# Kernel tuning notes

Measured on AMD Instinct MI355X. Metric: run time of the kernel, lower is better.

Reference implementation:

```python
import jax, jax.numpy as jnp
import numpy as np

B, T, D_IN = 8192, 32, 2
EMB, H = 128, 256


def setup_inputs() -> dict:
    key = jax.random.key(0)
    ks = jax.random.split(key, 8)
    s = 0.05
    return {
        "traj_inputs": jax.random.normal(ks[0], (B, T, D_IN), dtype=jnp.float32),
        "W_emb": jax.random.normal(ks[1], (D_IN, EMB), dtype=jnp.float32) * s,
        "b_emb": jnp.zeros((EMB,), dtype=jnp.float32),
        "W0": jax.random.normal(ks[2], (EMB, 4 * H), dtype=jnp.float32) * s,
        "U0": jax.random.normal(ks[3], (H, 4 * H), dtype=jnp.float32) * s,
        "b0": jnp.zeros((4 * H,), dtype=jnp.float32),
        "W1": jax.random.normal(ks[4], (H, 4 * H), dtype=jnp.float32) * s,
        "U1": jax.random.normal(ks[5], (H, 4 * H), dtype=jnp.float32) * s,
        "b1": jnp.zeros((4 * H,), dtype=jnp.float32),
    }


def _lstm_layer(x_seq, W, U, b):
    # x_seq: [B, T, D]; Keras LSTMCell gate order i, f, g(c), o
    bsz = x_seq.shape[0]
    h0 = jnp.zeros((bsz, H), dtype=x_seq.dtype)
    c0 = jnp.zeros((bsz, H), dtype=x_seq.dtype)
    # precompute input projection for all timesteps (one big GEMM)
    xz = jnp.einsum("btd,dk->btk", x_seq, W) + b  # [B, T, 4H]

    def step(carry, xz_t):
        h, c = carry
        z = xz_t + h @ U
        i, f, g, o = jnp.split(z, 4, axis=-1)
        i = jax.nn.sigmoid(i)
        f = jax.nn.sigmoid(f)
        g = jnp.tanh(g)
        o = jax.nn.sigmoid(o)
        c = f * c + i * g
        h = o * jnp.tanh(c)
        return (h, c), h

    (h_f, c_f), ys = jax.lax.scan(step, (h0, c0), jnp.swapaxes(xz, 0, 1))
    return jnp.swapaxes(ys, 0, 1), h_f, c_f  # [B,T,H], [B,H], [B,H]


def reference(traj_inputs, W_emb, b_emb, W0, U0, b0, W1, U1, b1):
    # position embedding: Dense(emb_size, relu)
    x = jax.nn.relu(traj_inputs @ W_emb + b_emb)  # [B, T, EMB]
    # stacked 2-layer LSTM, return_sequences + return_state
    y0, h0, c0 = _lstm_layer(x, W0, U0, b0)
    y1, h1, c1 = _lstm_layer(y0, W1, U1, b1)
    # Keras RNN(StackedRNNCells) returns (seq_out, [h0,c0], [h1,c1])
    return y1, h0, c0, h1, c1
```

## Files before the change

### kernel.cpp

```cpp
#include <hip/hip_runtime.h>
#include <hip/hip_bf16.h>


typedef __attribute__((ext_vector_type(8))) __bf16 bf16x8;
typedef __attribute__((ext_vector_type(4))) __bf16 bf16x4;
typedef __attribute__((ext_vector_type(4))) float f32x4;

#define MFMA16(a, b, c) __builtin_amdgcn_mfma_f32_16x16x32_bf16(a, b, c, 0, 0, 0)

#define WAIT_VM7() __builtin_amdgcn_s_waitcnt(0xF77)
#define WAIT_LGKM0() __builtin_amdgcn_s_waitcnt(0xC07F)
#define RAW_BARRIER()                  \
  do {                                 \
    WAIT_LGKM0();                      \
    __builtin_amdgcn_sched_barrier(0); \
    __builtin_amdgcn_s_barrier();      \
  } while (0)

__device__ __forceinline__ float fexp2(float x) {
#if __has_builtin(__builtin_amdgcn_exp2f)
  return __builtin_amdgcn_exp2f(x);
#else
  return exp2f(x);
#endif
}
__device__ __forceinline__ float frcp(float x) {
#if __has_builtin(__builtin_amdgcn_rcpf)
  return __builtin_amdgcn_rcpf(x);
#else
  return 1.0f / x;
#endif
}
__device__ __forceinline__ float fsig(float x) {
  return frcp(1.0f + fexp2(-1.44269504f * x));
}
__device__ __forceinline__ float ftanh(float x) {
  return 1.0f - 2.0f * frcp(1.0f + fexp2(2.88539008f * x));
}

__global__ void prep_w0(const float* __restrict__ W0, const float* __restrict__ U0,
                        __bf16* __restrict__ o) {
  const int f = blockIdx.x * 256 + threadIdx.x;
  const int j = f & 7, l5 = (f >> 3) & 63, g = f >> 9;
  const int kc = g % 12, q = (g / 12) & 3, wid = g / 48;
  const int k = (kc << 5) + ((l5 >> 4) << 3) + j;
  const int c = (q << 8) + ((wid >> 2) << 6) + ((wid & 3) << 4) + (l5 & 15);
  const float v = (k < 128) ? W0[(k << 10) + c] : U0[((k - 128) << 10) + c];
  o[f] = (__bf16)v;
}
__global__ void prep_w1(const float* __restrict__ W1, const float* __restrict__ U1,
                        __bf16* __restrict__ o) {
  const int f = blockIdx.x * 256 + threadIdx.x;
  const int j = f & 7, l5 = (f >> 3) & 63, g = f >> 9;
  const int kcx = g & 15, q = (g >> 4) & 3, wid = g >> 6;
  const int k = (kcx << 5) + ((l5 >> 4) << 3) + j;
  const int c = (q << 8) + ((wid >> 2) << 6) + ((wid & 3) << 4) + (l5 & 15);
  const float v = (k < 256) ? W1[(k << 10) + c] : U1[((k - 256) << 10) + c];
  o[f] = (__bf16)v;
}

__global__ __launch_bounds__(1024)
void lstm_l0(const float* __restrict__ traj,
             const float* __restrict__ Wemb,
             const float* __restrict__ bemb,
             const float* __restrict__ bias0,
             const __bf16* __restrict__ wb0,
             float* __restrict__ out,
             __bf16* __restrict__ slab) {
  __shared__ float s_We[384];
  __shared__ float s_traj[2048];
  __shared__ __bf16 s_h0[8192];
  __shared__ __bf16 s_ring[65536];

  const int tid = threadIdx.x;
  const int wid = tid >> 6;
  const int l = tid & 63;
  const int lr = l & 15, lg = l >> 4;
  const int w = wid >> 2, s4 = wid & 3;
  const int xr = (lr & 7) << 3;
  const int r0 = blockIdx.x << 5;
  const int e0 = (w << 6) + (s4 << 4) + (lg << 2);

  if (tid < 384) s_We[tid] = (tid < 256) ? Wemb[tid] : bemb[tid - 256];
  for (int i = tid; i < 2048; i += 1024) {
    const int r = i >> 6, tt = (i >> 1) & 31, d = i & 1;
    s_traj[(tt << 6) + (r << 1) + d] = traj[(r0 << 6) + i];
  }
  for (int i = tid; i < 8192; i += 1024) s_h0[i] = (__bf16)0.f;
  __syncthreads();

  float c0s[2][4] = {};
  const __bf16* wp0 = wb0 + wid * 48 * 512 + l * 8;
  __bf16* ringp = &s_ring[wid << 12];

  auto stage = [&](int cf) {
    const __bf16* src = wp0 + (((cf & 3) * 12 + (cf >> 2)) << 9);
    __builtin_amdgcn_global_load_lds(
        (const __attribute__((address_space(1))) void*)src,
        (__attribute__((address_space(3))) void*)(ringp + ((cf & 7) << 9)),
        16, 0, 0);
  };
  auto ring_read = [&](int cf) {
    return *reinterpret_cast<const bf16x8*>(ringp + ((cf & 7) << 9) + (l << 3));
  };

  stage(0); stage(1); stage(2); stage(3); stage(4); stage(5); stage(6);

#pragma unroll 1
  for (int t = 0; t < 32; ++t) {
    f32x4 acc[4][2];
#pragma unroll
    for (int q = 0; q < 4; ++q) {
      const f32x4 bq = *reinterpret_cast<const f32x4*>(bias0 + (q << 8) + e0);
      acc[q][0] = bq;
      acc[q][1] = bq;
    }
    float t0v[2], t1v[2];
#pragma unroll
    for (int rt = 0; rt < 2; ++rt) {
      const int r = (rt << 4) + lr;
      t0v[rt] = s_traj[(t << 6) + (r << 1)];
      t1v[rt] = s_traj[(t << 6) + (r << 1) + 1];
    }
#pragma unroll
    for (int kc = 0; kc < 12; ++kc) {
      bf16x8 ia[2];
      if (kc < 4) {
#pragma unroll
        for (int rt = 0; rt < 2; ++rt) {
#pragma unroll
          for (int j = 0; j < 8; ++j) {
            const int k = (kc << 5) + (lg << 3) + j;
            const float x = fmaf(t0v[rt], s_We[k],
                                 fmaf(t1v[rt], s_We[128 + k], s_We[256 + k]));
            ia[rt][j] = (__bf16)fmaxf(x, 0.f);
          }
        }
      } else {
#pragma unroll
        for (int rt = 0; rt < 2; ++rt) {
          const int r = (rt << 4) + lr;
          ia[rt] = *reinterpret_cast<const bf16x8*>(
              &s_h0[(r << 8) + ((((kc - 4) << 5) + (lg << 3)) ^ xr)]);
        }
      }
#pragma unroll
      for (int q = 0; q < 4; ++q) {
        const int cf = (kc << 2) + q;
        stage((cf + 7) % 48);
        WAIT_VM7();
        __builtin_amdgcn_sched_barrier(0);
        const bf16x8 wf = ring_read(cf);
        acc[q][0] = MFMA16(wf, ia[0], acc[q][0]);
        acc[q][1] = MFMA16(wf, ia[1], acc[q][1]);
      }
    }
    RAW_BARRIER();
#pragma unroll
    for (int rt = 0; rt < 2; ++rt) {
      const int r = (rt << 4) + lr;
      bf16x4 hv;
      f32x4 cfv;
#pragma unroll
      for (int i = 0; i < 4; ++i) {
        const float cc = fsig(acc[1][rt][i]) * c0s[rt][i] +
                         fsig(acc[0][rt][i]) * ftanh(acc[2][rt][i]);
        c0s[rt][i] = cc;
        hv[i] = (__bf16)(fsig(acc[3][rt][i]) * ftanh(cc));
        cfv[i] = cc;
      }
      *reinterpret_cast<bf16x4*>(&s_h0[(r << 8) + (e0 ^ xr)]) = hv;
      if (t == 31) {
        *reinterpret_cast<f32x4*>(out + 69206016 + ((r0 + r) << 8) + e0) = cfv;
      }
    }
    RAW_BARRIER();

#pragma unroll
    for (int rr = 0; rr < 2; ++rr) {
      const int row = (wid << 1) + rr;
      const bf16x4 hv4 = *reinterpret_cast<const bf16x4*>(
          &s_h0[(row << 8) + ((l << 2) ^ ((row & 7) << 3))]);
      *reinterpret_cast<bf16x4*>(
          slab + ((size_t)(t * 8192 + r0 + row) << 8) + (l << 2)) = hv4;
      if (t == 31) {
        f32x4 v;
#pragma unroll
        for (int i = 0; i < 4; ++i) v[i] = (float)hv4[i];
        *reinterpret_cast<f32x4*>(out + 67108864 + ((r0 + row) << 8) + (l << 2)) = v;
      }
    }
  }
}

__global__ __launch_bounds__(1024)
void lstm_l1(const float* __restrict__ bias1,
             const __bf16* __restrict__ wb1,
             const __bf16* __restrict__ slab,
             float* __restrict__ out) {
  __shared__ __bf16 s_h0[8192];
  __shared__ __bf16 s_h1[8192];
  __shared__ __bf16 s_ring[65536];

  const int tid = threadIdx.x;
  const int wid = tid >> 6;
  const int l = tid & 63;
  const int lr = l & 15, lg = l >> 4;
  const int w = wid >> 2, s4 = wid & 3;
  const int xr = (lr & 7) << 3;
  const int r0 = blockIdx.x << 5;
  const int e0 = (w << 6) + (s4 << 4) + (lg << 2);

  for (int i = tid; i < 8192; i += 1024) s_h1[i] = (__bf16)0.f;
  __syncthreads();

  float c1s[2][4] = {};
  const __bf16* wp1 = wb1 + wid * 64 * 512 + l * 8;
  __bf16* ringp = &s_ring[wid << 12];

  auto stage = [&](int cf) {
    const int it8 = (cf >> 2) & 15, q = cf & 3;
    const int kcx = it8 ^ 8;
    const __bf16* src = wp1 + (((q << 4) + kcx) << 9);
    __builtin_amdgcn_global_load_lds(
        (const __attribute__((address_space(1))) void*)src,
        (__attribute__((address_space(3))) void*)(ringp + ((cf & 7) << 9)),
        16, 0, 0);
  };
  auto ring_read = [&](int cf) {
    return *reinterpret_cast<const bf16x8*>(ringp + ((cf & 7) << 9) + (l << 3));
  };

  const int irow = (wid << 1) + (l >> 5);
  const int iwb = (l & 31) << 4;
  const size_t ioff =
      ((size_t)(r0 + irow) << 8) + ((iwb ^ ((irow & 7) << 4)) >> 1);

  stage(0); stage(1); stage(2); stage(3); stage(4); stage(5); stage(6);

#pragma unroll 1
  for (int t = 0; t < 32; ++t) {
    __builtin_amdgcn_global_load_lds(
        (const __attribute__((address_space(1))) void*)(slab +
            (((size_t)t * 8192) << 8) + ioff),
        (__attribute__((address_space(3))) void*)(s_h0 + (wid << 9)),
        16, 0, 0);

    f32x4 acc[4][2];
#pragma unroll
    for (int q = 0; q < 4; ++q) {
      const f32x4 bq = *reinterpret_cast<const f32x4*>(bias1 + (q << 8) + e0);
      acc[q][0] = bq;
      acc[q][1] = bq;
    }
#pragma unroll
    for (int it8 = 0; it8 < 8; ++it8) {
      bf16x8 ib[2];
#pragma unroll
      for (int rt = 0; rt < 2; ++rt) {
        const int r = (rt << 4) + lr;
        ib[rt] = *reinterpret_cast<const bf16x8*>(
            &s_h1[(r << 8) + (((it8 << 5) + (lg << 3)) ^ xr)]);
      }
#pragma unroll
      for (int q = 0; q < 4; ++q) {
        const int cf = (it8 << 2) + q;
        stage((cf + 7) % 64);
        WAIT_VM7();
        __builtin_amdgcn_sched_barrier(0);
        const bf16x8 wf = ring_read(cf);
        acc[q][0] = MFMA16(wf, ib[0], acc[q][0]);
        acc[q][1] = MFMA16(wf, ib[1], acc[q][1]);
      }
    }
    RAW_BARRIER();
#pragma unroll
    for (int it8 = 8; it8 < 16; ++it8) {
      const int kcl = it8 - 8;
      bf16x8 ib[2];
#pragma unroll
      for (int rt = 0; rt < 2; ++rt) {
        const int r = (rt << 4) + lr;
        ib[rt] = *reinterpret_cast<const bf16x8*>(
            &s_h0[(r << 8) + (((kcl << 5) + (lg << 3)) ^ xr)]);
      }
#pragma unroll
      for (int q = 0; q < 4; ++q) {
        const int cf = (it8 << 2) + q;
        stage((cf + 7) % 64);
        WAIT_VM7();
        __builtin_amdgcn_sched_barrier(0);
        const bf16x8 wf = ring_read(cf);
        acc[q][0] = MFMA16(wf, ib[0], acc[q][0]);
        acc[q][1] = MFMA16(wf, ib[1], acc[q][1]);
      }
    }
    RAW_BARRIER();
#pragma unroll
    for (int rt = 0; rt < 2; ++rt) {
      const int r = (rt << 4) + lr;
      bf16x4 hv;
      f32x4 cfv;
#pragma unroll
      for (int i = 0; i < 4; ++i) {
        const float cc = fsig(acc[1][rt][i]) * c1s[rt][i] +
                         fsig(acc[0][rt][i]) * ftanh(acc[2][rt][i]);
        c1s[rt][i] = cc;
        hv[i] = (__bf16)(fsig(acc[3][rt][i]) * ftanh(cc));
        cfv[i] = cc;
      }
      *reinterpret_cast<bf16x4*>(&s_h1[(r << 8) + (e0 ^ xr)]) = hv;
      if (t == 31) {
        *reinterpret_cast<f32x4*>(out + 73400320 + ((r0 + r) << 8) + e0) = cfv;
      }
    }
    RAW_BARRIER();

#pragma unroll
    for (int j = 0; j < 2; ++j) {
      const int row = (wid << 1) + j;
      const int xw = (row & 7) << 3;
      const bf16x4 a =
          *reinterpret_cast<const bf16x4*>(&s_h1[(row << 8) + ((l << 2) ^ xw)]);
      f32x4 v;
#pragma unroll
      for (int i = 0; i < 4; ++i) v[i] = (float)a[i];
      *reinterpret_cast<f32x4*>(out + ((((r0 + row) << 5) + t) << 8) + (l << 2)) = v;
      if (t == 31) {
        *reinterpret_cast<f32x4*>(out + 71303168 + ((r0 + row) << 8) + (l << 2)) = v;
      }
    }
  }
}

extern "C" void kernel_launch(void* const* d_in, const int* in_sizes, int n_in,
                              void* d_out, int out_size, void* d_ws, size_t ws_size,
                              hipStream_t stream) {
  const float* traj = (const float*)d_in[0];
  const float* Wemb = (const float*)d_in[1];
  const float* bemb = (const float*)d_in[2];
  const float* W0 = (const float*)d_in[3];
  const float* U0 = (const float*)d_in[4];
  const float* b0 = (const float*)d_in[5];
  const float* W1 = (const float*)d_in[6];
  const float* U1 = (const float*)d_in[7];
  const float* b1 = (const float*)d_in[8];
  float* out = (float*)d_out;

  __bf16* wb0 = (__bf16*)d_ws;
  __bf16* wb1 = wb0 + 393216;
  const size_t slab_off = 1835008;
  __bf16* slab = (__bf16*)((char*)d_ws + slab_off);

  hipLaunchKernelGGL(prep_w0, dim3(1536), dim3(256), 0, stream, W0, U0, wb0);
  hipLaunchKernelGGL(prep_w1, dim3(2048), dim3(256), 0, stream, W1, U1, wb1);
  hipLaunchKernelGGL(lstm_l0, dim3(256), dim3(1024), 0, stream,
                     traj, Wemb, bemb, b0, wb0, out, slab);
  hipLaunchKernelGGL(lstm_l1, dim3(256), dim3(1024), 0, stream,
                     b1, wb1, slab, out);
}
```

Baseline: 1.460 ms.

## Split LSTM batch into 16-row blocks of 512 threads for two blocks per CU

Each block of both LSTM kernels now handles 16 batch rows with 8 waves instead of 32 rows with 16 waves, and the grid doubles to 512 blocks. Each wave now covers two 16-column gate tiles for one row tile, so every weight fragment feeds one MFMA instead of two. The per-wave weight ring shrinks from 8 to 4 slots, with prefetch distance 3 and a matching waitcnt. The smaller LDS footprint and block size are meant to let two blocks share a CU and overlap their barrier and gate phases. The cost is that weights are streamed from cache twice as often overall, and the shallower prefetch leaves less latency hiding.

```diff
diff --git a/kernel.cpp b/kernel.cpp
--- a/kernel.cpp
+++ b/kernel.cpp
@@ -8,7 +8,7 @@
 
 #define MFMA16(a, b, c) __builtin_amdgcn_mfma_f32_16x16x32_bf16(a, b, c, 0, 0, 0)
 
-#define WAIT_VM7() __builtin_amdgcn_s_waitcnt(0xF77)
+#define WAIT_VM3() __builtin_amdgcn_s_waitcnt(0xF73)
 #define WAIT_LGKM0() __builtin_amdgcn_s_waitcnt(0xC07F)
 #define RAW_BARRIER()                  \
   do {                                 \
@@ -42,9 +42,9 @@
                         __bf16* __restrict__ o) {
   const int f = blockIdx.x * 256 + threadIdx.x;
   const int j = f & 7, l5 = (f >> 3) & 63, g = f >> 9;
-  const int kc = g % 12, q = (g / 12) & 3, wid = g / 48;
+  const int kc = g % 12, q = (g / 12) & 3, T = g / 48;
   const int k = (kc << 5) + ((l5 >> 4) << 3) + j;
-  const int c = (q << 8) + ((wid >> 2) << 6) + ((wid & 3) << 4) + (l5 & 15);
+  const int c = (q << 8) + ((T >> 2) << 6) + ((T & 3) << 4) + (l5 & 15);
   const float v = (k < 128) ? W0[(k << 10) + c] : U0[((k - 128) << 10) + c];
   o[f] = (__bf16)v;
 }
@@ -52,14 +52,14 @@
                         __bf16* __restrict__ o) {
   const int f = blockIdx.x * 256 + threadIdx.x;
   const int j = f & 7, l5 = (f >> 3) & 63, g = f >> 9;
-  const int kcx = g & 15, q = (g >> 4) & 3, wid = g >> 6;
+  const int kcx = g & 15, q = (g >> 4) & 3, T = g >> 6;
   const int k = (kcx << 5) + ((l5 >> 4) << 3) + j;
-  const int c = (q << 8) + ((wid >> 2) << 6) + ((wid & 3) << 4) + (l5 & 15);
+  const int c = (q << 8) + ((T >> 2) << 6) + ((T & 3) << 4) + (l5 & 15);
   const float v = (k < 256) ? W1[(k << 10) + c] : U1[((k - 256) << 10) + c];
   o[f] = (__bf16)v;
 }
 
-__global__ __launch_bounds__(1024)
+__global__ __launch_bounds__(512)
 void lstm_l0(const float* __restrict__ traj,
              const float* __restrict__ Wemb,
              const float* __restrict__ bemb,
@@ -68,110 +68,99 @@
              float* __restrict__ out,
              __bf16* __restrict__ slab) {
   __shared__ float s_We[384];
-  __shared__ float s_traj[2048];
-  __shared__ __bf16 s_h0[8192];
-  __shared__ __bf16 s_ring[65536];
+  __shared__ float s_traj[1024];
+  __shared__ __bf16 s_h0[4096];
+  __shared__ __bf16 s_ring[16384];
 
   const int tid = threadIdx.x;
   const int wid = tid >> 6;
   const int l = tid & 63;
   const int lr = l & 15, lg = l >> 4;
-  const int w = wid >> 2, s4 = wid & 3;
   const int xr = (lr & 7) << 3;
-  const int r0 = blockIdx.x << 5;
-  const int e0 = (w << 6) + (s4 << 4) + (lg << 2);
+  const int r0 = blockIdx.x << 4;
+  const int eT1 = ((wid >> 2) << 6) + ((wid & 3) << 4);
+  const int e0a = eT1 + (lg << 2);
+  const int e0b = e0a + 128;
 
   if (tid < 384) s_We[tid] = (tid < 256) ? Wemb[tid] : bemb[tid - 256];
-  for (int i = tid; i < 2048; i += 1024) {
+  for (int i = tid; i < 1024; i += 512) {
     const int r = i >> 6, tt = (i >> 1) & 31, d = i & 1;
-    s_traj[(tt << 6) + (r << 1) + d] = traj[(r0 << 6) + i];
+    s_traj[(tt << 5) + (r << 1) + d] = traj[(r0 << 6) + i];
   }
-  for (int i = tid; i < 8192; i += 1024) s_h0[i] = (__bf16)0.f;
+  for (int i = tid; i < 4096; i += 512) s_h0[i] = (__bf16)0.f;
   __syncthreads();
 
   float c0s[2][4] = {};
-  const __bf16* wp0 = wb0 + wid * 48 * 512 + l * 8;
-  __bf16* ringp = &s_ring[wid << 12];
+  __bf16* ringp = &s_ring[wid << 11];
 
   auto stage = [&](int cf) {
-    const __bf16* src = wp0 + (((cf & 3) * 12 + (cf >> 2)) << 9);
+    const int kc = cf >> 3, tile2 = (cf >> 2) & 1, q = cf & 3;
+    const __bf16* src =
+        wb0 + (((wid + (tile2 << 3)) * 48 + q * 12 + kc) << 9) + (l << 3);
     __builtin_amdgcn_global_load_lds(
         (const __attribute__((address_space(1))) void*)src,
-        (__attribute__((address_space(3))) void*)(ringp + ((cf & 7) << 9)),
+        (__attribute__((address_space(3))) void*)(ringp + ((cf & 3) << 9)),
         16, 0, 0);
   };
   auto ring_read = [&](int cf) {
-    return *reinterpret_cast<const bf16x8*>(ringp + ((cf & 7) << 9) + (l << 3));
+    return *reinterpret_cast<const bf16x8*>(ringp + ((cf & 3) << 9) + (l << 3));
   };
 
-  stage(0); stage(1); stage(2); stage(3); stage(4); stage(5); stage(6);
+  stage(0); stage(1); stage(2);
 
 #pragma unroll 1
   for (int t = 0; t < 32; ++t) {
     f32x4 acc[4][2];
 #pragma unroll
     for (int q = 0; q < 4; ++q) {
-      const f32x4 bq = *reinterpret_cast<const f32x4*>(bias0 + (q << 8) + e0);
-      acc[q][0] = bq;
-      acc[q][1] = bq;
-    }
-    float t0v[2], t1v[2];
-#pragma unroll
-    for (int rt = 0; rt < 2; ++rt) {
-      const int r = (rt << 4) + lr;
-      t0v[rt] = s_traj[(t << 6) + (r << 1)];
-      t1v[rt] = s_traj[(t << 6) + (r << 1) + 1];
-    }
+      acc[q][0] = *reinterpret_cast<const f32x4*>(bias0 + (q << 8) + e0a);
+      acc[q][1] = *reinterpret_cast<const f32x4*>(bias0 + (q << 8) + e0b);
+    }
+    const float t0v = s_traj[(t << 5) + (lr << 1)];
+    const float t1v = s_traj[(t << 5) + (lr << 1) + 1];
 #pragma unroll
     for (int kc = 0; kc < 12; ++kc) {
-      bf16x8 ia[2];
+      bf16x8 ia;
       if (kc < 4) {
 #pragma unroll
-        for (int rt = 0; rt < 2; ++rt) {
-#pragma unroll
-          for (int j = 0; j < 8; ++j) {
-            const int k = (kc << 5) + (lg << 3) + j;
-            const float x = fmaf(t0v[rt], s_We[k],
-                                 fmaf(t1v[rt], s_We[128 + k], s_We[256 + k]));
-            ia[rt][j] = (__bf16)fmaxf(x, 0.f);
-          }
+        for (int j = 0; j < 8; ++j) {
+          const int k = (kc << 5) + (lg << 3) + j;
+          const float x =
+              fmaf(t0v, s_We[k], fmaf(t1v, s_We[128 + k], s_We[256 + k]));
+          ia[j] = (__bf16)fmaxf(x, 0.f);
         }
       } else {
-#pragma unroll
-        for (int rt = 0; rt < 2; ++rt) {
-          const int r = (rt << 4) + lr;
-          ia[rt] = *reinterpret_cast<const bf16x8*>(
-              &s_h0[(r << 8) + ((((kc - 4) << 5) + (lg << 3)) ^ xr)]);
-        }
-      }
-#pragma unroll
-      for (int q = 0; q < 4; ++q) {
-        const int cf = (kc << 2) + q;
-        stage((cf + 7) % 48);
-        WAIT_VM7();
+        ia = *reinterpret_cast<const bf16x8*>(
+            &s_h0[(lr << 8) + ((((kc - 4) << 5) + (lg << 3)) ^ xr)]);
+      }
+#pragma unroll
+      for (int c8 = 0; c8 < 8; ++c8) {
+        const int cf = (kc << 3) + c8;
+        const int tile2 = (cf >> 2) & 1, q = cf & 3;
+        stage((cf + 3) % 96);
+        WAIT_VM3();
         __builtin_amdgcn_sched_barrier(0);
         const bf16x8 wf = ring_read(cf);
-        acc[q][0] = MFMA16(wf, ia[0], acc[q][0]);
-        acc[q][1] = MFMA16(wf, ia[1], acc[q][1]);
-      }
-    }
-    RAW_BARRIER();
-#pragma unroll
-    for (int rt = 0; rt < 2; ++rt) {
-      const int r = (rt << 4) + lr;
+        acc[q][tile2] = MFMA16(wf, ia, acc[q][tile2]);
+      }
+    }
+    RAW_BARRIER();
+#pragma unroll
+    for (int tile2 = 0; tile2 < 2; ++tile2) {
+      const int e0 = tile2 ? e0b : e0a;
       bf16x4 hv;
       f32x4 cfv;
 #pragma unroll
       for (int i = 0; i < 4; ++i) {
-        const float cc = fsig(acc[1][rt][i]) * c0s[rt][i] +
-                         fsig(acc[0][rt][i]) * ftanh(acc[2][rt][i]);
-        c0s[rt][i] = cc;
-        hv[i] = (__bf16)(fsig(acc[3][rt][i]) * ftanh(cc));
+        const float cc = fsig(acc[1][tile2][i]) * c0s[tile2][i] +
+                         fsig(acc[0][tile2][i]) * ftanh(acc[2][tile2][i]);
+        c0s[tile2][i] = cc;
+        hv[i] = (__bf16)(fsig(acc[3][tile2][i]) * ftanh(cc));
         cfv[i] = cc;
       }
-      *reinterpret_cast<bf16x4*>(&s_h0[(r << 8) + (e0 ^ xr)]) = hv;
+      *reinterpret_cast<bf16x4*>(&s_h0[(lr << 8) + (e0 ^ xr)]) = hv;
       if (t == 31) {
-        *reinterpret_cast<f32x4*>(out + 69206016 + ((r0 + r) << 8) + e0) = cfv;
+        *reinterpret_cast<f32x4*>(out + 69206016 + ((r0 + lr) << 8) + e0) = cfv;
       }
     }
     RAW_BARRIER();
@@ -193,42 +182,43 @@
   }
 }
 
-__global__ __launch_bounds__(1024)
+__global__ __launch_bounds__(512)
 void lstm_l1(const float* __restrict__ bias1,
              const __bf16* __restrict__ wb1,
              const __bf16* __restrict__ slab,
              float* __restrict__ out) {
-  __shared__ __bf16 s_h0[8192];
-  __shared__ __bf16 s_h1[8192];
-  __shared__ __bf16 s_ring[65536];
+  __shared__ __bf16 s_h0[4096];
+  __shared__ __bf16 s_h1[4096];
+  __shared__ __bf16 s_ring[16384];
 
   const int tid = threadIdx.x;
   const int wid = tid >> 6;
   const int l = tid & 63;
   const int lr = l & 15, lg = l >> 4;
-  const int w = wid >> 2, s4 = wid & 3;
   const int xr = (lr & 7) << 3;
-  const int r0 = blockIdx.x << 5;
-  const int e0 = (w << 6) + (s4 << 4) + (lg << 2);
-
-  for (int i = tid; i < 8192; i += 1024) s_h1[i] = (__bf16)0.f;
+  const int r0 = blockIdx.x << 4;
+  const int eT1 = ((wid >> 2) << 6) + ((wid & 3) << 4);
+  const int e0a = eT1 + (lg << 2);
+  const int e0b = e0a + 128;
+
+  for (int i = tid; i < 4096; i += 512) s_h1[i] = (__bf16)0.f;
   __syncthreads();
 
   float c1s[2][4] = {};
-  const __bf16* wp1 = wb1 + wid * 64 * 512 + l * 8;
-  __bf16* ringp = &s_ring[wid << 12];
+  __bf16* ringp = &s_ring[wid << 11];
 
   auto stage = [&](int cf) {
-    const int it8 = (cf >> 2) & 15, q = cf & 3;
+    const int it8 = (cf >> 3) & 15, tile2 = (cf >> 2) & 1, q = cf & 3;
     const int kcx = it8 ^ 8;
-    const __bf16* src = wp1 + (((q << 4) + kcx) << 9);
+    const __bf16* src =
+        wb1 + (((wid + (tile2 << 3)) * 64 + (q << 4) + kcx) << 9) + (l << 3);
     __builtin_amdgcn_global_load_lds(
         (const __attribute__((address_space(1))) void*)src,
-        (__attribute__((address_space(3))) void*)(ringp + ((cf & 7) << 9)),
+        (__attribute__((address_space(3))) void*)(ringp + ((cf & 3) << 9)),
         16, 0, 0);
   };
   auto ring_read = [&](int cf) {
-    return *reinterpret_cast<const bf16x8*>(ringp + ((cf & 7) << 9) + (l << 3));
+    return *reinterpret_cast<const bf16x8*>(ringp + ((cf & 3) << 9) + (l << 3));
   };
 
   const int irow = (wid << 1) + (l >> 5);
@@ -236,7 +226,7 @@
   const size_t ioff =
       ((size_t)(r0 + irow) << 8) + ((iwb ^ ((irow & 7) << 4)) >> 1);
 
-  stage(0); stage(1); stage(2); stage(3); stage(4); stage(5); stage(6);
+  stage(0); stage(1); stage(2);
 
 #pragma unroll 1
   for (int t = 0; t < 32; ++t) {
@@ -249,69 +239,58 @@
     f32x4 acc[4][2];
 #pragma unroll
     for (int q = 0; q < 4; ++q) {
-      const f32x4 bq = *reinterpret_cast<const f32x4*>(bias1 + (q << 8) + e0);
-      acc[q][0] = bq;
-      acc[q][1] = bq;
+      acc[q][0] = *reinterpret_cast<const f32x4*>(bias1 + (q << 8) + e0a);
+      acc[q][1] = *reinterpret_cast<const f32x4*>(bias1 + (q << 8) + e0b);
     }
 #pragma unroll
     for (int it8 = 0; it8 < 8; ++it8) {
-      bf16x8 ib[2];
-#pragma unroll
-      for (int rt = 0; rt < 2; ++rt) {
-        const int r = (rt << 4) + lr;
-        ib[rt] = *reinterpret_cast<const bf16x8*>(
-            &s_h1[(r << 8) + (((it8 << 5) + (lg << 3)) ^ xr)]);
-      }
-#pragma unroll
-      for (int q = 0; q < 4; ++q) {
-        const int cf = (it8 << 2) + q;
-        stage((cf + 7) % 64);
-        WAIT_VM7();
+      const bf16x8 ib = *reinterpret_cast<const bf16x8*>(
+          &s_h1[(lr << 8) + (((it8 << 5) + (lg << 3)) ^ xr)]);
+#pragma unroll
+      for (int c8 = 0; c8 < 8; ++c8) {
+        const int cf = (it8 << 3) + c8;
+        const int tile2 = (cf >> 2) & 1, q = cf & 3;
+        stage((cf + 3) % 128);
+        WAIT_VM3();
         __builtin_amdgcn_sched_barrier(0);
         const bf16x8 wf = ring_read(cf);
-        acc[q][0] = MFMA16(wf, ib[0], acc[q][0]);
-        acc[q][1] = MFMA16(wf, ib[1], acc[q][1]);
+        acc[q][tile2] = MFMA16(wf, ib, acc[q][tile2]);
       }
     }
     RAW_BARRIER();
 #pragma unroll
     for (int it8 = 8; it8 < 16; ++it8) {
       const int kcl = it8 - 8;
-      bf16x8 ib[2];
-#pragma unroll
-      for (int rt = 0; rt < 2; ++rt) {
-        const int r = (rt << 4) + lr;
-        ib[rt] = *reinterpret_cast<const bf16x8*>(
-            &s_h0[(r << 8) + (((kcl << 5) + (lg << 3)) ^ xr)]);
-      }
-#pragma unroll
-      for (int q = 0; q < 4; ++q) {
-        const int cf = (it8 << 2) + q;
-        stage((cf + 7) % 64);
-        WAIT_VM7();
+      const bf16x8 ib = *reinterpret_cast<const bf16x8*>(
+          &s_h0[(lr << 8) + (((kcl << 5) + (lg << 3)) ^ xr)]);
+#pragma unroll
+      for (int c8 = 0; c8 < 8; ++c8) {
+        const int cf = (it8 << 3) + c8;
+        const int tile2 = (cf >> 2) & 1, q = cf & 3;
+        stage((cf + 3) % 128);
+        WAIT_VM3();
         __builtin_amdgcn_sched_barrier(0);
         const bf16x8 wf = ring_read(cf);
-        acc[q][0] = MFMA16(wf, ib[0], acc[q][0]);
-        acc[q][1] = MFMA16(wf, ib[1], acc[q][1]);
-      }
-    }
-    RAW_BARRIER();
-#pragma unroll
-    for (int rt = 0; rt < 2; ++rt) {
-      const int r = (rt << 4) + lr;
+        acc[q][tile2] = MFMA16(wf, ib, acc[q][tile2]);
+      }
+    }
+    RAW_BARRIER();
+#pragma unroll
+    for (int tile2 = 0; tile2 < 2; ++tile2) {
+      const int e0 = tile2 ? e0b : e0a;
       bf16x4 hv;
       f32x4 cfv;
 #pragma unroll
       for (int i = 0; i < 4; ++i) {
-        const float cc = fsig(acc[1][rt][i]) * c1s[rt][i] +
-                         fsig(acc[0][rt][i]) * ftanh(acc[2][rt][i]);
-        c1s[rt][i] = cc;
-        hv[i] = (__bf16)(fsig(acc[3][rt][i]) * ftanh(cc));
+        const float cc = fsig(acc[1][tile2][i]) * c1s[tile2][i] +
+                         fsig(acc[0][tile2][i]) * ftanh(acc[2][tile2][i]);
+        c1s[tile2][i] = cc;
+        hv[i] = (__bf16)(fsig(acc[3][tile2][i]) * ftanh(cc));
         cfv[i] = cc;
       }
-      *reinterpret_cast<bf16x4*>(&s_h1[(r << 8) + (e0 ^ xr)]) = hv;
+      *reinterpret_cast<bf16x4*>(&s_h1[(lr << 8) + (e0 ^ xr)]) = hv;
       if (t == 31) {
-        *reinterpret_cast<f32x4*>(out + 73400320 + ((r0 + r) << 8) + e0) = cfv;
+        *reinterpret_cast<f32x4*>(out + 73400320 + ((r0 + lr) << 8) + e0) = cfv;
       }
     }
     RAW_BARRIER();
@@ -354,8 +333,8 @@
 
   hipLaunchKernelGGL(prep_w0, dim3(1536), dim3(256), 0, stream, W0, U0, wb0);
   hipLaunchKernelGGL(prep_w1, dim3(2048), dim3(256), 0, stream, W1, U1, wb1);
-  hipLaunchKernelGGL(lstm_l0, dim3(256), dim3(1024), 0, stream,
+  hipLaunchKernelGGL(lstm_l0, dim3(512), dim3(512), 0, stream,
                      traj, Wemb, bemb, b0, wb0, out, slab);
-  hipLaunchKernelGGL(lstm_l1, dim3(256), dim3(1024), 0, stream,
+  hipLaunchKernelGGL(lstm_l1, dim3(512), dim3(512), 0, stream,
                      b1, wb1, slab, out);
 }
```

New measurement: 2.652 ms. 81.7% more time.
